# Kernel tuning notes

Hardware: AMD Instinct MI355X
Metric: run time of the kernel (lower is better)

## Reference

```python
import jax, jax.numpy as jnp
import numpy as np

DIM = 1536
HEADS = 12
HEAD_DIM = 128
SEQ = 3120
FRAME = 1560
EPS = 1e-6


def _rmsnorm(x, gamma, eps=EPS):
    var = jnp.mean(jnp.square(x), axis=-1, keepdims=True)
    return x * jax.lax.rsqrt(var + eps) * gamma


def _rope(x, cos, sin):
    # x: [B,S,H,D], cos/sin: [S, D//2]; rotate interleaved pairs (Wan-style)
    xr = x.reshape(x.shape[:-1] + (x.shape[-1] // 2, 2))
    x1, x2 = xr[..., 0], xr[..., 1]
    c = cos[None, :, None, :]
    s = sin[None, :, None, :]
    o1 = x1 * c - x2 * s
    o2 = x1 * s + x2 * c
    return jnp.stack([o1, o2], axis=-1).reshape(x.shape)


def setup_inputs() -> dict:
    key = jax.random.key(0)
    ks = jax.random.split(key, 8)
    pos = jnp.arange(SEQ, dtype=jnp.float32)[:, None]
    inv_freq = 1.0 / (10000.0 ** (jnp.arange(0, HEAD_DIM // 2, dtype=jnp.float32) / (HEAD_DIM // 2)))
    ang = pos * inv_freq[None, :]
    return {
        "hidden_states": jax.random.normal(ks[0], (1, SEQ, DIM), jnp.float32),
        "freqs_cos": jnp.cos(ang),
        "freqs_sin": jnp.sin(ang),
        "w_qkv": jax.random.normal(ks[1], (DIM, 3 * DIM), jnp.float32) * (DIM ** -0.5),
        "b_qkv": jnp.zeros((3 * DIM,), jnp.float32),
        "g_q": jnp.ones((DIM,), jnp.float32),
        "g_k": jnp.ones((DIM,), jnp.float32),
        "w_out": jax.random.normal(ks[2], (DIM, DIM), jnp.float32) * (DIM ** -0.5),
        "b_out": jnp.zeros((DIM,), jnp.float32),
        "frame_len": FRAME,
    }


def reference(hidden_states, freqs_cos, freqs_sin, w_qkv, b_qkv, g_q, g_k, w_out, b_out, frame_len):
    B, S, _ = hidden_states.shape
    qkv = hidden_states @ w_qkv + b_qkv  # [B,S,3*DIM]
    q, k, v = jnp.split(qkv, 3, axis=-1)
    q = _rmsnorm(q, g_q)
    k = _rmsnorm(k, g_k)
    q = q.reshape(B, S, HEADS, HEAD_DIM)
    k = k.reshape(B, S, HEADS, HEAD_DIM)
    v = v.reshape(B, S, HEADS, HEAD_DIM)
    q = _rope(q, freqs_cos, freqs_sin)
    k = _rope(k, freqs_cos, freqs_sin)
    # block-wise causal mask over frames of frame_len tokens
    blk = jnp.arange(S) // frame_len
    mask = blk[None, :] <= blk[:, None]  # [Sq, Sk]
    scale = 1.0 / jnp.sqrt(jnp.float32(HEAD_DIM))
    scores = jnp.einsum("bqhd,bkhd->bhqk", q, k) * scale
    scores = jnp.where(mask[None, None], scores, jnp.float32(-1e30))
    probs = jax.nn.softmax(scores, axis=-1)
    out = jnp.einsum("bhqk,bkhd->bqhd", probs, v)
    out = out.reshape(B, S, HEADS * HEAD_DIM)
    return out @ w_out + b_out
```

## Files before the change

### kernel.cpp

```cpp
#include <hip/hip_runtime.h>
#include <hip/hip_bf16.h>
#include <stdint.h>

#define SEQ_LEN 3120
#define DIM 1536
#define QKV_N 4608
#define HEADS 12
#define HEAD_DIM 128
#define FRAME_LEN 1560
#define SM_SCALE 0.08838834764831845f
#define LOG2E 1.4426950408889634f
#define FMAXC2 43.280851226669165f
#define BQ 256

#if __has_builtin(__builtin_amdgcn_exp2f)
#define FEXP2(x) __builtin_amdgcn_exp2f(x)
#else
#define FEXP2(x) exp2f(x)
#endif

typedef short short8 __attribute__((ext_vector_type(8)));
typedef float f32x4 __attribute__((ext_vector_type(4)));
typedef float f32x16 __attribute__((ext_vector_type(16)));

__device__ __forceinline__ unsigned short f2bf(float x) {
    union { float f; unsigned u; } v; v.f = x;
    unsigned r = v.u + 0x7fffu + ((v.u >> 16) & 1u);
    return (unsigned short)(r >> 16);
}
__device__ __forceinline__ float bf2f(unsigned short b) {
    union { unsigned u; float f; } v; v.u = ((unsigned)b) << 16;
    return v.f;
}
__device__ __forceinline__ unsigned pk2bf(float a, float b) {
    __hip_bfloat162 h = __float22bfloat162_rn(make_float2(a, b));
    union { __hip_bfloat162 h2; unsigned u; } v; v.h2 = h;
    return v.u;
}

__device__ __forceinline__ void async16(void* lds, const void* g) {
    __builtin_amdgcn_global_load_lds(
        (const __attribute__((address_space(1))) unsigned int*)g,
        (__attribute__((address_space(3))) unsigned int*)lds, 16, 0, 0);
}

__device__ __forceinline__ void transpose_tile(
    const float* __restrict__ in, unsigned short* __restrict__ out,
    int R, int C, int c0, int r0, float (*T)[65], int tid)
{
    const int rl = tid >> 4, cl = (tid & 15) * 4;
#pragma unroll
    for (int i = 0; i < 4; ++i) {
        const int row = r0 + rl + i * 16;
        float4 v = *(const float4*)&in[(size_t)row * C + c0 + cl];
        T[cl + 0][rl + i * 16] = v.x; T[cl + 1][rl + i * 16] = v.y;
        T[cl + 2][rl + i * 16] = v.z; T[cl + 3][rl + i * 16] = v.w;
    }
    __syncthreads();
    const int oc = tid >> 2, ob = (tid & 3) * 16;
    union { unsigned short t[16]; uint4 u[2]; } p;
#pragma unroll
    for (int j = 0; j < 16; ++j) p.t[j] = f2bf(T[oc][ob + j]);
    uint4* dst = (uint4*)&out[(size_t)(c0 + oc) * R + r0 + ob];
    dst[0] = p.u[0];
    dst[1] = p.u[1];
}

__global__ __launch_bounds__(256) void prep_kernel(
    const float* __restrict__ hs, unsigned short* __restrict__ hsb,
    const float* __restrict__ w_qkv, unsigned short* __restrict__ wqkvT,
    const float* __restrict__ w_out, unsigned short* __restrict__ woutT)
{
    __shared__ float T[64][65];
    const int bid = blockIdx.x;
    const int tid = threadIdx.x;
    if (bid < 2340) {
        const int i = bid * 256 + tid;
        const float4 a = ((const float4*)hs)[i * 2];
        const float4 b = ((const float4*)hs)[i * 2 + 1];
        union { unsigned short t[8]; uint4 u; } p;
        p.t[0] = f2bf(a.x); p.t[1] = f2bf(a.y); p.t[2] = f2bf(a.z); p.t[3] = f2bf(a.w);
        p.t[4] = f2bf(b.x); p.t[5] = f2bf(b.y); p.t[6] = f2bf(b.z); p.t[7] = f2bf(b.w);
        ((uint4*)hsb)[i] = p.u;
    } else if (bid < 4068) {
        const int t = bid - 2340;
        transpose_tile(w_qkv, wqkvT, DIM, QKV_N, (t % 72) * 64, (t / 72) * 64, T, tid);
    } else {
        const int t = bid - 4068;
        transpose_tile(w_out, woutT, DIM, DIM, (t % 24) * 64, (t / 24) * 64, T, tid);
    }
}

__global__ __launch_bounds__(256, 2) void gemm_bt_kernel(
    const unsigned short* __restrict__ A, const unsigned short* __restrict__ Bt,
    const float* __restrict__ bias, float* __restrict__ C, int M, int N, int K,
    int ntp, int spx)
{
    __shared__ short As[128 * 32];
    __shared__ short Bs[128 * 32];

    const int xcd = blockIdx.x & 7;
    const int idx = (xcd & 1) * spx + (blockIdx.x >> 3);
    const int mtiles = (M + 127) >> 7;
    if (idx >= ntp * mtiles) return;
    const int m0 = (idx / ntp) * 128;
    const int n0 = ((xcd >> 1) * ntp + idx % ntp) * 128;

    const int tid = threadIdx.x;
    const int w = tid >> 6, l = tid & 63;
    const int wr = w >> 1, wc = w & 1;
    const int lhi = l >> 4, llo = l & 15;

    f32x4 acc[4][4];
#pragma unroll
    for (int i = 0; i < 4; ++i)
#pragma unroll
        for (int j = 0; j < 4; ++j) acc[i][j] = f32x4{0.f, 0.f, 0.f, 0.f};

    const int c0i = (w * 2) * 64 + l, c1i = c0i + 64;
    const unsigned short* gA0 = A + (size_t)min(m0 + (c0i >> 2), M - 1) * K + (c0i & 3) * 8;
    const unsigned short* gA1 = A + (size_t)min(m0 + (c1i >> 2), M - 1) * K + (c1i & 3) * 8;
    const unsigned short* gB0 = Bt + (size_t)(n0 + (c0i >> 2)) * K + (c0i & 3) * 8;
    const unsigned short* gB1 = Bt + (size_t)(n0 + (c1i >> 2)) * K + (c1i & 3) * 8;
    short* lA0 = As + (w * 2 + 0) * 512;
    short* lA1 = As + (w * 2 + 1) * 512;
    short* lB0 = Bs + (w * 2 + 0) * 512;
    short* lB1 = Bs + (w * 2 + 1) * 512;

    const int aoff = (wr * 64 + llo) * 32 + lhi * 8;
    const int boff = (wc * 64 + llo) * 32 + lhi * 8;

    for (int k0 = 0; k0 < K; k0 += 32) {
        async16(lA0, gA0 + k0); async16(lA1, gA1 + k0);
        async16(lB0, gB0 + k0); async16(lB1, gB1 + k0);
        __syncthreads();
        short8 af[4], bf[4];
#pragma unroll
        for (int mt = 0; mt < 4; ++mt) af[mt] = *(const short8*)&As[aoff + mt * 512];
#pragma unroll
        for (int nt = 0; nt < 4; ++nt) bf[nt] = *(const short8*)&Bs[boff + nt * 512];
#pragma unroll
        for (int mt = 0; mt < 4; ++mt)
#pragma unroll
            for (int nt = 0; nt < 4; ++nt)
                acc[mt][nt] = __builtin_amdgcn_mfma_f32_16x16x32_bf16(af[mt], bf[nt], acc[mt][nt], 0, 0, 0);
        __syncthreads();
    }

#pragma unroll
    for (int mt = 0; mt < 4; ++mt)
#pragma unroll
        for (int ri = 0; ri < 4; ++ri) {
            const int row = m0 + wr * 64 + mt * 16 + lhi * 4 + ri;
            if (row < M) {
#pragma unroll
                for (int nt = 0; nt < 4; ++nt) {
                    const int col = n0 + wc * 64 + nt * 16 + llo;
                    C[(size_t)row * N + col] = acc[mt][nt][ri] + bias[col];
                }
            }
        }
}

__global__ __launch_bounds__(256, 2) void gemm_bt_bf16_kernel(
    const unsigned short* __restrict__ A, const unsigned short* __restrict__ Bt,
    const float* __restrict__ bias, unsigned short* __restrict__ C, int M, int N, int K,
    int ntp, int spx)
{
    __shared__ short As[128 * 32];
    __shared__ short Bs[128 * 32];

    const int xcd = blockIdx.x & 7;
    const int idx = (xcd & 1) * spx + (blockIdx.x >> 3);
    const int mtiles = (M + 127) >> 7;
    if (idx >= ntp * mtiles) return;
    const int m0 = (idx / ntp) * 128;
    const int n0 = ((xcd >> 1) * ntp + idx % ntp) * 128;

    const int tid = threadIdx.x;
    const int w = tid >> 6, l = tid & 63;
    const int wr = w >> 1, wc = w & 1;
    const int lhi = l >> 4, llo = l & 15;

    f32x4 acc[4][4];
#pragma unroll
    for (int i = 0; i < 4; ++i)
#pragma unroll
        for (int j = 0; j < 4; ++j) acc[i][j] = f32x4{0.f, 0.f, 0.f, 0.f};

    const int c0i = (w * 2) * 64 + l, c1i = c0i + 64;
    const unsigned short* gA0 = A + (size_t)min(m0 + (c0i >> 2), M - 1) * K + (c0i & 3) * 8;
    const unsigned short* gA1 = A + (size_t)min(m0 + (c1i >> 2), M - 1) * K + (c1i & 3) * 8;
    const unsigned short* gB0 = Bt + (size_t)(n0 + (c0i >> 2)) * K + (c0i & 3) * 8;
    const unsigned short* gB1 = Bt + (size_t)(n0 + (c1i >> 2)) * K + (c1i & 3) * 8;
    short* lA0 = As + (w * 2 + 0) * 512;
    short* lA1 = As + (w * 2 + 1) * 512;
    short* lB0 = Bs + (w * 2 + 0) * 512;
    short* lB1 = Bs + (w * 2 + 1) * 512;

    const int aoff = (wr * 64 + llo) * 32 + lhi * 8;
    const int boff = (wc * 64 + llo) * 32 + lhi * 8;

    for (int k0 = 0; k0 < K; k0 += 32) {
        async16(lA0, gA0 + k0); async16(lA1, gA1 + k0);
        async16(lB0, gB0 + k0); async16(lB1, gB1 + k0);
        __syncthreads();
        short8 af[4], bf[4];
#pragma unroll
        for (int mt = 0; mt < 4; ++mt) af[mt] = *(const short8*)&As[aoff + mt * 512];
#pragma unroll
        for (int nt = 0; nt < 4; ++nt) bf[nt] = *(const short8*)&Bs[boff + nt * 512];
#pragma unroll
        for (int mt = 0; mt < 4; ++mt)
#pragma unroll
            for (int nt = 0; nt < 4; ++nt)
                acc[mt][nt] = __builtin_amdgcn_mfma_f32_16x16x32_bf16(af[mt], bf[nt], acc[mt][nt], 0, 0, 0);
        __syncthreads();
    }

#pragma unroll
    for (int mt = 0; mt < 4; ++mt)
#pragma unroll
        for (int ri = 0; ri < 4; ++ri) {
            const int row = m0 + wr * 64 + mt * 16 + lhi * 4 + ri;
            if (row < M) {
#pragma unroll
                for (int nt = 0; nt < 4; ++nt) {
                    const int col = n0 + wc * 64 + nt * 16 + llo;
                    C[(size_t)row * N + col] = f2bf(acc[mt][nt][ri] + bias[col]);
                }
            }
        }
}

__global__ __launch_bounds__(256) void rmsrope_kernel(
    const unsigned short* __restrict__ qkvb, const float* __restrict__ gq,
    const float* __restrict__ gk, const float* __restrict__ cosf,
    const float* __restrict__ sinf, unsigned short* __restrict__ qb,
    unsigned short* __restrict__ kb)
{
    const int s = blockIdx.x;
    const int tid = threadIdx.x;
    const unsigned short* qrow = qkvb + (size_t)s * QKV_N;
    const unsigned short* krow = qrow + DIM;

    float2 qp[3], kp[3];
    float ssq_q = 0.f, ssq_k = 0.f;
#pragma unroll
    for (int j = 0; j < 3; ++j) {
        const int p = tid + j * 256;
        const unsigned uq = *(const unsigned*)(qrow + 2 * p);
        const unsigned uk = *(const unsigned*)(krow + 2 * p);
        qp[j] = make_float2(bf2f((unsigned short)(uq & 0xffff)), bf2f((unsigned short)(uq >> 16)));
        kp[j] = make_float2(bf2f((unsigned short)(uk & 0xffff)), bf2f((unsigned short)(uk >> 16)));
        ssq_q += qp[j].x * qp[j].x + qp[j].y * qp[j].y;
        ssq_k += kp[j].x * kp[j].x + kp[j].y * kp[j].y;
    }
#pragma unroll
    for (int off = 32; off > 0; off >>= 1) {
        ssq_q += __shfl_down(ssq_q, off);
        ssq_k += __shfl_down(ssq_k, off);
    }
    __shared__ float wq[4], wk[4];
    const int wave = tid >> 6, lane = tid & 63;
    if (lane == 0) { wq[wave] = ssq_q; wk[wave] = ssq_k; }
    __syncthreads();
    const float tq = wq[0] + wq[1] + wq[2] + wq[3];
    const float tk = wk[0] + wk[1] + wk[2] + wk[3];
    const float inv_q = rsqrtf(tq * (1.0f / DIM) + 1e-6f) * (SM_SCALE * LOG2E);
    const float inv_k = rsqrtf(tk * (1.0f / DIM) + 1e-6f);

#pragma unroll
    for (int j = 0; j < 3; ++j) {
        const int p = tid + j * 256;
        const int fi = p & 63;
        const float c = cosf[s * 64 + fi];
        const float si = sinf[s * 64 + fi];
        {
            const float y1 = qp[j].x * inv_q * gq[2 * p];
            const float y2 = qp[j].y * inv_q * gq[2 * p + 1];
            *(unsigned*)&qb[(size_t)s * DIM + 2 * p] = pk2bf(y1 * c - y2 * si, y1 * si + y2 * c);
        }
        {
            const float y1 = kp[j].x * inv_k * gk[2 * p];
            const float y2 = kp[j].y * inv_k * gk[2 * p + 1];
            *(unsigned*)&kb[(size_t)s * DIM + 2 * p] = pk2bf(y1 * c - y2 * si, y1 * si + y2 * c);
        }
    }
}

__global__ __launch_bounds__(256) void vtrans_kernel(
    const unsigned short* __restrict__ qkvb, unsigned short* __restrict__ vt)
{
    __shared__ float T[128][65];
    const int s0 = blockIdx.x * 64;
    const int h = blockIdx.y;
    const int tid = threadIdx.x;
    const int rl = tid >> 2, cb = (tid & 3) * 32;
    const int row = min(s0 + rl, SEQ_LEN - 1);
#pragma unroll
    for (int i = 0; i < 4; ++i) {
        const int d = cb + i * 8;
        union { uint4 u; unsigned short t[8]; } v;
        v.u = *(const uint4*)&qkvb[(size_t)row * QKV_N + 2 * DIM + h * HEAD_DIM + d];
#pragma unroll
        for (int j = 0; j < 8; ++j) T[d + j][rl] = bf2f(v.t[j]);
    }
    __syncthreads();
    const int od = tid >> 1, ob = (tid & 1) * 32;
    const size_t orow = (size_t)(h * HEAD_DIM + od) * SEQ_LEN;
#pragma unroll
    for (int v8 = 0; v8 < 4; ++v8) {
        const int s = s0 + ob + v8 * 8;
        if (s < SEQ_LEN) {
            union { unsigned short t[8]; uint4 u; } pk;
#pragma unroll
            for (int j = 0; j < 8; ++j) pk.t[j] = f2bf(T[od][ob + v8 * 8 + j]);
            *(uint4*)&vt[orow + s] = pk.u;
        }
    }
}

__global__ __launch_bounds__(512, 2) void attn_part_kernel(
    const unsigned short* __restrict__ qb, const unsigned short* __restrict__ kb,
    const unsigned short* __restrict__ vt, unsigned short* __restrict__ part_o,
    float* __restrict__ part_ml)
{
    __shared__ short KV[40960];

    const int bid = blockIdx.x;
    const int xcd = bid & 7;
    const int slot = bid >> 3;
    int h, bx;
    if (slot < 20) { h = xcd; bx = slot; }
    else { h = 8 + (xcd >> 1); bx = (xcd & 1) * 10 + (slot - 20); }

    const int tid = threadIdx.x;
    const int w = tid >> 6;
    const int l = tid & 63;
    int tile, split, nsp;
    if (bx < 6) { tile = bx; split = 0; nsp = 1; }
    else { const int b2 = bx - 6; tile = 6 + (b2 >> 1); split = b2 & 1; nsp = 2; }
    const int q0 = tile * BQ;
    const int lhi = l >> 5;
    const int llo = l & 31;

#pragma unroll
    for (int s = 0; s < 8; ++s) {
        const int c = (s * 8 + w) * 64 + l;
        const int row = c >> 4, g = c & 15;
        const int gr = min(q0 + row, SEQ_LEN - 1);
        async16(KV + (s * 8 + w) * 512, qb + (size_t)gr * DIM + h * HEAD_DIM + g * 8);
    }
    __syncthreads();
    short8 qf[8];
#pragma unroll
    for (int ds = 0; ds < 8; ++ds)
        qf[ds] = *(const short8*)&KV[(w * 32 + llo) * 128 + ds * 16 + lhi * 8];
    __syncthreads();

    const int myq = q0 + w * 32 + llo;
    const int mylimit = (myq < FRAME_LEN) ? FRAME_LEN : SEQ_LEN;
    const int wave_lim = (q0 + w * 32 < FRAME_LEN) ? FRAME_LEN : SEQ_LEN;
    const int Lmax = (tile < 6) ? FRAME_LEN : SEQ_LEN;
    const int nch = (Lmax + 63) >> 6;
    const int kc0 = ((split * nch) / nsp) * 64;
    const int kc1 = (((split + 1) * nch) / nsp) * 64;
    const int nchunks = (kc1 - kc0) >> 6;

    float l_run = 0.f;
    f32x16 o[4];
#pragma unroll
    for (int mt = 0; mt < 4; ++mt)
#pragma unroll
        for (int r = 0; r < 16; ++r) o[mt][r] = 0.f;

    int krloc[2], kcol[2], vcol[2], lof[2];
    size_t vrow[2];
#pragma unroll
    for (int s = 0; s < 2; ++s) {
        const int c = (s * 8 + w) * 64 + l;
        const int kr = c >> 4;
        krloc[s] = kr;
        kcol[s] = h * HEAD_DIM + (((c & 15) ^ (kr & 7)) * 8);
        const int d = c >> 3;
        vrow[s] = (size_t)(h * HEAD_DIM + d) * SEQ_LEN;
        vcol[s] = ((c & 7) ^ (d & 7)) * 8;
        lof[s] = (s * 8 + w) * 512;
    }

    auto issueK = [&](int kc, int b) {
#pragma unroll
        for (int s = 0; s < 2; ++s) {
            const int gr = min(kc + krloc[s], SEQ_LEN - 1);
            async16(KV + b * 8192 + lof[s], kb + (size_t)gr * DIM + kcol[s]);
        }
    };
    auto issueV = [&](int kc, int t) {
#pragma unroll
        for (int s = 0; s < 2; ++s) {
            const int col = min(kc + vcol[s], SEQ_LEN - 8);
            async16(KV + 16384 + t * 8192 + lof[s], vt + vrow[s] + col);
        }
    };

    auto qkt = [&](f32x16* st, int b) {
        const short* Kb = KV + b * 8192;
#pragma unroll
        for (int r = 0; r < 16; ++r) { st[0][r] = 0.f; st[1][r] = 0.f; }
#pragma unroll
        for (int ds = 0; ds < 8; ++ds) {
            const int gd = ds * 2 + lhi;
#pragma unroll
            for (int kt = 0; kt < 2; ++kt) {
                const int krow = kt * 32 + llo;
                short8 kf = *(const short8*)&Kb[krow * 128 + ((gd ^ (krow & 7)) * 8)];
                st[kt] = __builtin_amdgcn_mfma_f32_32x32x16_bf16(kf, qf[ds], st[kt], 0, 0, 0);
            }
        }
    };

    auto sm_pv = [&](f32x16* st, int kc, int t) {
        if (kc + 64 > wave_lim) {
#pragma unroll
            for (int kt = 0; kt < 2; ++kt)
#pragma unroll
                for (int r = 0; r < 16; ++r) {
                    const int kg = kc + kt * 32 + (r & 3) + 8 * (r >> 2) + 4 * lhi;
                    if (kg >= mylimit) st[kt][r] = -3.0e38f;
                }
        }
        float rs = 0.f;
        unsigned p16[2][8];
#pragma unroll
        for (int kt = 0; kt < 2; ++kt)
#pragma unroll
            for (int r2 = 0; r2 < 8; ++r2) {
                const float p0 = FEXP2(st[kt][2 * r2] - FMAXC2);
                const float p1 = FEXP2(st[kt][2 * r2 + 1] - FMAXC2);
                rs += p0 + p1;
                p16[kt][r2] = pk2bf(p0, p1);
            }
        l_run += rs;

        const short* Vb = KV + 16384 + t * 8192;
#pragma unroll
        for (int kblk = 0; kblk < 4; ++kblk) {
            const int tt = kblk >> 1;
            const int dk    = ((kblk & 1) * 2 + lhi) * 2;
            const int dsend = ((kblk & 1) * 2 + (1 - lhi)) * 2;
            const unsigned r0 = __shfl_xor(p16[tt][dsend], 32);
            const unsigned r1 = __shfl_xor(p16[tt][dsend + 1], 32);
            union { unsigned u[4]; short8 s8; } pf;
            if (lhi == 0) { pf.u[0] = p16[tt][dk]; pf.u[1] = p16[tt][dk + 1]; pf.u[2] = r0; pf.u[3] = r1; }
            else          { pf.u[0] = r0; pf.u[1] = r1; pf.u[2] = p16[tt][dk]; pf.u[3] = p16[tt][dk + 1]; }
#pragma unroll
            for (int mt = 0; mt < 4; ++mt) {
                const int vd = mt * 32 + llo;
                short8 vf = *(const short8*)&Vb[vd * 64 + (((kblk * 2 + lhi) ^ (vd & 7)) * 8)];
                o[mt] = __builtin_amdgcn_mfma_f32_32x32x16_bf16(vf, pf.s8, o[mt], 0, 0, 0);
            }
        }
    };

    issueK(kc0, 0); issueV(kc0, 0);
    if (nchunks > 1) { issueK(kc0 + 64, 1); issueV(kc0 + 64, 1); }
    __syncthreads();
    f32x16 stC[2];
    qkt(stC, 0);

    int vcur = 0;
    for (int i = 0, kc = kc0; i < nchunks; ++i, kc += 64) {
        __syncthreads();
        if (i + 2 < nchunks) {
            issueK(kc + 128, i & 1);
            int vt2 = vcur + 2; if (vt2 >= 3) vt2 -= 3;
            issueV(kc + 128, vt2);
        }
        f32x16 stN[2];
        if (i + 1 < nchunks) qkt(stN, (i + 1) & 1);
        sm_pv(stC, kc, vcur);
        if (i + 1 < nchunks) { stC[0] = stN[0]; stC[1] = stN[1]; }
        vcur = (vcur == 2) ? 0 : vcur + 1;
    }

    const float l_tot = l_run + __shfl_xor(l_run, 32);
    const int slot_o = bx * HEADS + h;
    const int qloc = w * 32 + llo;
    const float inv = (l_tot > 0.f) ? 1.0f / l_tot : 0.f;
    unsigned short* op = part_o + (size_t)slot_o * (BQ * HEAD_DIM) + qloc * HEAD_DIM + 4 * lhi;
#pragma unroll
    for (int mt = 0; mt < 4; ++mt)
#pragma unroll
        for (int g = 0; g < 4; ++g) {
            uint2 u;
            u.x = pk2bf(o[mt][4 * g + 0] * inv, o[mt][4 * g + 1] * inv);
            u.y = pk2bf(o[mt][4 * g + 2] * inv, o[mt][4 * g + 3] * inv);
            *(uint2*)&op[mt * 32 + 8 * g] = u;
        }
    if (lhi == 0) part_ml[(size_t)slot_o * BQ + qloc] = l_tot;
}

__global__ __launch_bounds__(256) void attn_combine_kernel(
    const unsigned short* __restrict__ part_o, const float* __restrict__ part_ml,
    unsigned short* __restrict__ attb)
{
    const int h = blockIdx.y;
    const int q = blockIdx.x * 8 + (threadIdx.x >> 5);
    const int dq = (threadIdx.x & 31) * 4;
    const int tile = q >> 8, qloc = q & 255;
    int base_bx, ns;
    if (tile < 6) { base_bx = tile; ns = 1; }
    else { base_bx = 6 + (tile - 6) * 2; ns = 2; }

    float W = 0.f;
    float acc[4] = {0.f, 0.f, 0.f, 0.f};
    for (int s = 0; s < ns; ++s) {
        const int slot = (base_bx + s) * HEADS + h;
        const float w = part_ml[(size_t)slot * BQ + qloc];
        if (w > 0.f) {
            W += w;
            const unsigned short* po = part_o +
                (size_t)slot * (BQ * HEAD_DIM) + qloc * HEAD_DIM + dq;
            uint2 u = *(const uint2*)po;
            acc[0] += w * bf2f((unsigned short)(u.x & 0xffff));
            acc[1] += w * bf2f((unsigned short)(u.x >> 16));
            acc[2] += w * bf2f((unsigned short)(u.y & 0xffff));
            acc[3] += w * bf2f((unsigned short)(u.y >> 16));
        }
    }
    const float inv = 1.0f / W;
    uint2 pk;
    pk.x = pk2bf(acc[0] * inv, acc[1] * inv);
    pk.y = pk2bf(acc[2] * inv, acc[3] * inv);
    *(uint2*)&attb[(size_t)q * DIM + h * HEAD_DIM + dq] = pk;
}

extern "C" void kernel_launch(void* const* d_in, const int* in_sizes, int n_in,
                              void* d_out, int out_size, void* d_ws, size_t ws_size,
                              hipStream_t stream)
{
    const float* hs    = (const float*)d_in[0];
    const float* cosf  = (const float*)d_in[1];
    const float* sinf  = (const float*)d_in[2];
    const float* w_qkv = (const float*)d_in[3];
    const float* b_qkv = (const float*)d_in[4];
    const float* g_q   = (const float*)d_in[5];
    const float* g_k   = (const float*)d_in[6];
    const float* w_out = (const float*)d_in[7];
    const float* b_out = (const float*)d_in[8];

    char* base = (char*)d_ws;
    unsigned short* qb     = (unsigned short*)base;
    unsigned short* kb     = (unsigned short*)(base + 9584640);
    unsigned short* vt     = (unsigned short*)(base + 19169280);
    unsigned short* hsb    = vt;
    unsigned short* qkvb   = (unsigned short*)(base + 28753920);
    unsigned short* part_o = (unsigned short*)(base + 28753920);
    float*          part_ml= (float*)(base + 60211200);
    unsigned short* wqkvT  = (unsigned short*)(base + 81469440);
    unsigned short* attb   = wqkvT;
    unsigned short* woutT  = (unsigned short*)(base + 95625216);
    float* outp = (float*)d_out;

    prep_kernel<<<4644, 256, 0, stream>>>(hs, hsb, w_qkv, wqkvT, w_out, woutT);
    gemm_bt_bf16_kernel<<<904, 256, 0, stream>>>(
        hsb, wqkvT, b_qkv, qkvb, SEQ_LEN, QKV_N, DIM, 9, 113);
    rmsrope_kernel<<<SEQ_LEN, 256, 0, stream>>>(qkvb, g_q, g_k, cosf, sinf, qb, kb);
    vtrans_kernel<<<dim3((SEQ_LEN + 63) / 64, HEADS), 256, 0, stream>>>(qkvb, vt);
    attn_part_kernel<<<240, 512, 0, stream>>>(qb, kb, vt, part_o, part_ml);
    attn_combine_kernel<<<dim3(SEQ_LEN / 8, HEADS), 256, 0, stream>>>(part_o, part_ml, attb);
    gemm_bt_kernel<<<304, 256, 0, stream>>>(
        attb, woutT, b_out, outp, SEQ_LEN, DIM, DIM, 3, 38);
}
```

Measured before the change: 328.0 us.

## Double-buffer GEMM LDS tiles and use permlane32 swap for P fragments

Both GEMM kernels now keep two LDS buffers, issuing the async load of the next K tile before computing on the current one. This cuts the loop to one barrier per iteration and overlaps global-to-LDS traffic with MFMA work. The attention kernel also replaces the shuffle-based exchange of bf16 probability halves between lane groups with the permlane32_swap builtin when it is available. That avoids ds_bpermute traffic and per-lane select logic. The cost is doubled LDS use per GEMM block, which could limit occupancy.

```diff
diff --git a/kernel.cpp b/kernel.cpp
--- a/kernel.cpp
+++ b/kernel.cpp
@@ -96,8 +96,8 @@
     const float* __restrict__ bias, float* __restrict__ C, int M, int N, int K,
     int ntp, int spx)
 {
-    __shared__ short As[128 * 32];
-    __shared__ short Bs[128 * 32];
+    __shared__ short As[2][4096];
+    __shared__ short Bs[2][4096];
 
     const int xcd = blockIdx.x & 7;
     const int idx = (xcd & 1) * spx + (blockIdx.x >> 3);
@@ -122,29 +122,34 @@
     const unsigned short* gA1 = A + (size_t)min(m0 + (c1i >> 2), M - 1) * K + (c1i & 3) * 8;
     const unsigned short* gB0 = Bt + (size_t)(n0 + (c0i >> 2)) * K + (c0i & 3) * 8;
     const unsigned short* gB1 = Bt + (size_t)(n0 + (c1i >> 2)) * K + (c1i & 3) * 8;
-    short* lA0 = As + (w * 2 + 0) * 512;
-    short* lA1 = As + (w * 2 + 1) * 512;
-    short* lB0 = Bs + (w * 2 + 0) * 512;
-    short* lB1 = Bs + (w * 2 + 1) * 512;
 
     const int aoff = (wr * 64 + llo) * 32 + lhi * 8;
     const int boff = (wc * 64 + llo) * 32 + lhi * 8;
 
-    for (int k0 = 0; k0 < K; k0 += 32) {
-        async16(lA0, gA0 + k0); async16(lA1, gA1 + k0);
-        async16(lB0, gB0 + k0); async16(lB1, gB1 + k0);
+    auto stage = [&](int k0, int b) {
+        async16(As[b] + (w * 2 + 0) * 512, gA0 + k0);
+        async16(As[b] + (w * 2 + 1) * 512, gA1 + k0);
+        async16(Bs[b] + (w * 2 + 0) * 512, gB0 + k0);
+        async16(Bs[b] + (w * 2 + 1) * 512, gB1 + k0);
+    };
+
+    const int nk = K >> 5;
+    stage(0, 0);
+    for (int t = 0; t < nk; ++t) {
         __syncthreads();
+        if (t + 1 < nk) stage((t + 1) * 32, (t + 1) & 1);
+        const short* A_ = As[t & 1];
+        const short* B_ = Bs[t & 1];
         short8 af[4], bf[4];
 #pragma unroll
-        for (int mt = 0; mt < 4; ++mt) af[mt] = *(const short8*)&As[aoff + mt * 512];
-#pragma unroll
-        for (int nt = 0; nt < 4; ++nt) bf[nt] = *(const short8*)&Bs[boff + nt * 512];
+        for (int mt = 0; mt < 4; ++mt) af[mt] = *(const short8*)&A_[aoff + mt * 512];
+#pragma unroll
+        for (int nt = 0; nt < 4; ++nt) bf[nt] = *(const short8*)&B_[boff + nt * 512];
 #pragma unroll
         for (int mt = 0; mt < 4; ++mt)
 #pragma unroll
             for (int nt = 0; nt < 4; ++nt)
                 acc[mt][nt] = __builtin_amdgcn_mfma_f32_16x16x32_bf16(af[mt], bf[nt], acc[mt][nt], 0, 0, 0);
-        __syncthreads();
     }
 
 #pragma unroll
@@ -167,8 +172,8 @@
     const float* __restrict__ bias, unsigned short* __restrict__ C, int M, int N, int K,
     int ntp, int spx)
 {
-    __shared__ short As[128 * 32];
-    __shared__ short Bs[128 * 32];
+    __shared__ short As[2][4096];
+    __shared__ short Bs[2][4096];
 
     const int xcd = blockIdx.x & 7;
     const int idx = (xcd & 1) * spx + (blockIdx.x >> 3);
@@ -193,29 +198,34 @@
     const unsigned short* gA1 = A + (size_t)min(m0 + (c1i >> 2), M - 1) * K + (c1i & 3) * 8;
     const unsigned short* gB0 = Bt + (size_t)(n0 + (c0i >> 2)) * K + (c0i & 3) * 8;
     const unsigned short* gB1 = Bt + (size_t)(n0 + (c1i >> 2)) * K + (c1i & 3) * 8;
-    short* lA0 = As + (w * 2 + 0) * 512;
-    short* lA1 = As + (w * 2 + 1) * 512;
-    short* lB0 = Bs + (w * 2 + 0) * 512;
-    short* lB1 = Bs + (w * 2 + 1) * 512;
 
     const int aoff = (wr * 64 + llo) * 32 + lhi * 8;
     const int boff = (wc * 64 + llo) * 32 + lhi * 8;
 
-    for (int k0 = 0; k0 < K; k0 += 32) {
-        async16(lA0, gA0 + k0); async16(lA1, gA1 + k0);
-        async16(lB0, gB0 + k0); async16(lB1, gB1 + k0);
+    auto stage = [&](int k0, int b) {
+        async16(As[b] + (w * 2 + 0) * 512, gA0 + k0);
+        async16(As[b] + (w * 2 + 1) * 512, gA1 + k0);
+        async16(Bs[b] + (w * 2 + 0) * 512, gB0 + k0);
+        async16(Bs[b] + (w * 2 + 1) * 512, gB1 + k0);
+    };
+
+    const int nk = K >> 5;
+    stage(0, 0);
+    for (int t = 0; t < nk; ++t) {
         __syncthreads();
+        if (t + 1 < nk) stage((t + 1) * 32, (t + 1) & 1);
+        const short* A_ = As[t & 1];
+        const short* B_ = Bs[t & 1];
         short8 af[4], bf[4];
 #pragma unroll
-        for (int mt = 0; mt < 4; ++mt) af[mt] = *(const short8*)&As[aoff + mt * 512];
-#pragma unroll
-        for (int nt = 0; nt < 4; ++nt) bf[nt] = *(const short8*)&Bs[boff + nt * 512];
+        for (int mt = 0; mt < 4; ++mt) af[mt] = *(const short8*)&A_[aoff + mt * 512];
+#pragma unroll
+        for (int nt = 0; nt < 4; ++nt) bf[nt] = *(const short8*)&B_[boff + nt * 512];
 #pragma unroll
         for (int mt = 0; mt < 4; ++mt)
 #pragma unroll
             for (int nt = 0; nt < 4; ++nt)
                 acc[mt][nt] = __builtin_amdgcn_mfma_f32_16x16x32_bf16(af[mt], bf[nt], acc[mt][nt], 0, 0, 0);
-        __syncthreads();
     }
 
 #pragma unroll
@@ -447,13 +457,27 @@
 #pragma unroll
         for (int kblk = 0; kblk < 4; ++kblk) {
             const int tt = kblk >> 1;
-            const int dk    = ((kblk & 1) * 2 + lhi) * 2;
-            const int dsend = ((kblk & 1) * 2 + (1 - lhi)) * 2;
-            const unsigned r0 = __shfl_xor(p16[tt][dsend], 32);
-            const unsigned r1 = __shfl_xor(p16[tt][dsend + 1], 32);
+            const int i0 = (kblk & 1) * 4;
             union { unsigned u[4]; short8 s8; } pf;
-            if (lhi == 0) { pf.u[0] = p16[tt][dk]; pf.u[1] = p16[tt][dk + 1]; pf.u[2] = r0; pf.u[3] = r1; }
-            else          { pf.u[0] = r0; pf.u[1] = r1; pf.u[2] = p16[tt][dk]; pf.u[3] = p16[tt][dk + 1]; }
+#if __has_builtin(__builtin_amdgcn_permlane32_swap)
+            {
+                auto s02 = __builtin_amdgcn_permlane32_swap(
+                    p16[tt][i0 + 0], p16[tt][i0 + 2], false, false);
+                auto s13 = __builtin_amdgcn_permlane32_swap(
+                    p16[tt][i0 + 1], p16[tt][i0 + 3], false, false);
+                pf.u[0] = s02[0]; pf.u[1] = s13[0];
+                pf.u[2] = s02[1]; pf.u[3] = s13[1];
+            }
+#else
+            {
+                const int dk    = ((kblk & 1) * 2 + lhi) * 2;
+                const int dsend = ((kblk & 1) * 2 + (1 - lhi)) * 2;
+                const unsigned r0 = __shfl_xor(p16[tt][dsend], 32);
+                const unsigned r1 = __shfl_xor(p16[tt][dsend + 1], 32);
+                if (lhi == 0) { pf.u[0] = p16[tt][dk]; pf.u[1] = p16[tt][dk + 1]; pf.u[2] = r0; pf.u[3] = r1; }
+                else          { pf.u[0] = r0; pf.u[1] = r1; pf.u[2] = p16[tt][dk]; pf.u[3] = p16[tt][dk + 1]; }
+            }
+#endif
 #pragma unroll
             for (int mt = 0; mt < 4; ++mt) {
                 const int vd = mt * 32 + llo;
```

Measured after the change: 296.4 us. 1.11x faster.
